# Performance work log

Hardware: AMD Instinct MI355X
Metric: run time of the kernel (lower is better)

The kernel has to match this reference:

```python
import jax, jax.numpy as jnp
import numpy as np

N = 8192
IN_F = 256
OUT_F = 64
ALPHA = 0.2
NEG_INF = -9e15


def setup_inputs() -> dict:
    key = jax.random.key(0)
    k1, k2, k3, k4 = jax.random.split(key, 4)
    h = jax.random.normal(k1, (N, IN_F), dtype=jnp.float32)
    W = jax.random.normal(k2, (IN_F, OUT_F), dtype=jnp.float32) * (1.414 / np.sqrt(IN_F))
    a = jax.random.normal(k3, (2 * OUT_F, 1), dtype=jnp.float32) * (1.414 / np.sqrt(2 * OUT_F))
    adj = jax.random.randint(k4, (N, N), 0, 2, dtype=jnp.int32)
    return {"h": h, "W": W, "a": a, "adj": adj}


def reference(h, W, a, adj):
    # Wh: [N, F]
    Wh = h @ W
    # Decompose concat-based attention: e_ij = LeakyReLU(Wh_i . a[:F] + Wh_j . a[F:])
    a1, a2 = a[:OUT_F], a[OUT_F:]
    src = Wh @ a1              # [N, 1] contribution of row i
    dst = Wh @ a2              # [N, 1] contribution of col j
    e = jax.nn.leaky_relu(src + dst.T, negative_slope=ALPHA)  # [N, N]
    e = jnp.where(adj > 0, e, NEG_INF)
    attention = jax.nn.softmax(e, axis=1)
    # dropout is identity in eval mode
    h_prime = attention @ Wh   # [N, F]
    return h_prime
```

## Files before the change

kernel.cpp:

```cpp
#include <hip/hip_runtime.h>

#define NROWS 8192
#define NSPLIT 8
#define JT (NROWS / NSPLIT)
#define NITER (JT / 64)
#define L2E 1.4426950408889634f

typedef __attribute__((ext_vector_type(4))) float f32x4;
typedef __attribute__((ext_vector_type(8))) __bf16 bf16x8;
typedef __attribute__((ext_vector_type(4))) unsigned int u32x4;

__device__ __forceinline__ unsigned short f2bf(float x) {
  unsigned u = __float_as_uint(x);
  u += 0x7fffu + ((u >> 16) & 1u);
  return (unsigned short)(u >> 16);
}

__global__ __launch_bounds__(256) void k_prep(
    const float* __restrict__ h, const float* __restrict__ W,
    const float* __restrict__ a, unsigned short* __restrict__ WhB,
    float* __restrict__ src, float* __restrict__ dst) {
  int i = blockIdx.x * 4 + (threadIdx.x >> 6);
  int lane = threadIdx.x & 63;
  const float* hrow = h + (size_t)i * 256;
  float s = 0.f;
#pragma unroll 4
  for (int k = 0; k < 256; k += 4) {
    float4 hv = *(const float4*)(hrow + k);
    s = fmaf(hv.x, W[(k + 0) * 64 + lane], s);
    s = fmaf(hv.y, W[(k + 1) * 64 + lane], s);
    s = fmaf(hv.z, W[(k + 2) * 64 + lane], s);
    s = fmaf(hv.w, W[(k + 3) * 64 + lane], s);
  }
  int nt = lane >> 4, c = lane & 15;
  int gi = (i >> 3) & 3, e = i & 7;
  int idx = ((((i >> 5) * 4 + nt) * 64) + c + 16 * gi) * 8 + e;
  WhB[idx] = f2bf(s);
  float v1 = s * a[lane];
  float v2 = s * a[64 + lane];
#pragma unroll
  for (int d = 32; d; d >>= 1) {
    v1 += __shfl_xor(v1, d);
    v2 += __shfl_xor(v2, d);
  }
  if (lane == 0) {
    src[i] = v1 * L2E;
    dst[i] = v2 * L2E;
  }
}

__global__ __launch_bounds__(256) void k_dmax(
    const float* __restrict__ dst, float* __restrict__ dmax) {
  __shared__ float red[4];
  float v = -INFINITY;
  for (int i = threadIdx.x; i < NROWS; i += 256) v = fmaxf(v, dst[i]);
#pragma unroll
  for (int d = 32; d; d >>= 1) v = fmaxf(v, __shfl_xor(v, d));
  if ((threadIdx.x & 63) == 0) red[threadIdx.x >> 6] = v;
  __syncthreads();
  if (threadIdx.x == 0)
    *dmax = fmaxf(fmaxf(red[0], red[1]), fmaxf(red[2], red[3]));
}

__global__ __launch_bounds__(256, 4) void k_attn(
    const int* __restrict__ adj, const unsigned short* __restrict__ WhB,
    const float* __restrict__ src, const float* __restrict__ dst,
    const float* __restrict__ dmax,
    float* __restrict__ pl, float* __restrict__ pacc) {
  __shared__ float ldst[JT];
  int task = blockIdx.x * 4 + (threadIdx.x >> 6);
  int sp = task >> 9;
  int mt = task & 511;
  int lane = threadIdx.x & 63;
  int r = lane & 15;
  int g = lane >> 4;
  int row0 = mt * 16;
  int jbase = sp * JT;

  for (int k = threadIdx.x; k < JT; k += 256) ldst[k] = dst[jbase + k];
  __syncthreads();

  float srcr = src[row0 + r];
  float dmv = *dmax;
  float vB = srcr + dmv;
  float Mi = fmaxf(vB, 0.2f * vB);

  float lrow = 0.f;
  f32x4 acc[4] = {f32x4{0.f, 0.f, 0.f, 0.f}, f32x4{0.f, 0.f, 0.f, 0.f},
                  f32x4{0.f, 0.f, 0.f, 0.f}, f32x4{0.f, 0.f, 0.f, 0.f}};
  const int* adjp = adj + (size_t)(row0 + r) * NROWS + jbase + 8 * g;
  const bf16x8* Bfr = (const bf16x8*)WhB;

  int4 ab[2][4];
  ab[0][0] = *(const int4*)(adjp + 0);
  ab[0][1] = *(const int4*)(adjp + 4);
  ab[0][2] = *(const int4*)(adjp + 32);
  ab[0][3] = *(const int4*)(adjp + 36);

#pragma unroll
  for (int it = 0; it < NITER; ++it) {
    const int jb = it * 64;
    const int cur = it & 1, nxt = cur ^ 1;

    int jc = (jbase + jb) >> 5;
    const bf16x8* bp = Bfr + (size_t)jc * 256 + lane;
    bf16x8 b0 = bp[0];
    bf16x8 b1 = bp[64];
    bf16x8 b2 = bp[128];
    bf16x8 b3 = bp[192];
    bf16x8 b4 = bp[256];
    bf16x8 b5 = bp[320];
    bf16x8 b6 = bp[384];
    bf16x8 b7 = bp[448];
    __builtin_amdgcn_sched_barrier(0);

    const int* ap = adjp + ((it < NITER - 1) ? jb + 64 : 0);
    ab[nxt][0] = *(const int4*)(ap + 0);
    ab[nxt][1] = *(const int4*)(ap + 4);
    ab[nxt][2] = *(const int4*)(ap + 32);
    ab[nxt][3] = *(const int4*)(ap + 36);
    __builtin_amdgcn_sched_barrier(0);

    const float4* dl = (const float4*)(ldst + jb + 8 * g);
    float4 d0 = dl[0];
    float4 d1 = dl[1];
    const float4* dl2 = (const float4*)(ldst + jb + 32 + 8 * g);
    float4 d2 = dl2[0];
    float4 d3 = dl2[1];

    float p[16];
#define PE(P, AA, DD)                     \
  {                                       \
    float v_ = srcr + (DD);               \
    v_ = fmaxf(v_, 0.2f * v_);            \
    float e_ = exp2f(v_ - Mi);            \
    (P) = ((AA) > 0) ? e_ : 0.f;          \
  }
    PE(p[0], ab[cur][0].x, d0.x) PE(p[1], ab[cur][0].y, d0.y)
    PE(p[2], ab[cur][0].z, d0.z) PE(p[3], ab[cur][0].w, d0.w)
    PE(p[4], ab[cur][1].x, d1.x) PE(p[5], ab[cur][1].y, d1.y)
    PE(p[6], ab[cur][1].z, d1.z) PE(p[7], ab[cur][1].w, d1.w)
    PE(p[8], ab[cur][2].x, d2.x) PE(p[9], ab[cur][2].y, d2.y)
    PE(p[10], ab[cur][2].z, d2.z) PE(p[11], ab[cur][2].w, d2.w)
    PE(p[12], ab[cur][3].x, d3.x) PE(p[13], ab[cur][3].y, d3.y)
    PE(p[14], ab[cur][3].z, d3.z) PE(p[15], ab[cur][3].w, d3.w)
#undef PE

    unsigned q[8];
#pragma unroll
    for (int t = 0; t < 16; t += 2) {
      lrow += p[t] + p[t + 1];
      unsigned qq;
      asm("v_cvt_pk_bf16_f32 %0, %1, %2" : "=v"(qq) : "v"(p[t]), "v"(p[t + 1]));
      q[t >> 1] = qq;
    }
    u32x4 qv0 = {q[0], q[1], q[2], q[3]};
    u32x4 qv1 = {q[4], q[5], q[6], q[7]};
    bf16x8 A0 = __builtin_bit_cast(bf16x8, qv0);
    bf16x8 A1 = __builtin_bit_cast(bf16x8, qv1);

    __builtin_amdgcn_s_setprio(1);
    acc[0] = __builtin_amdgcn_mfma_f32_16x16x32_bf16(A0, b0, acc[0], 0, 0, 0);
    acc[1] = __builtin_amdgcn_mfma_f32_16x16x32_bf16(A0, b1, acc[1], 0, 0, 0);
    acc[2] = __builtin_amdgcn_mfma_f32_16x16x32_bf16(A0, b2, acc[2], 0, 0, 0);
    acc[3] = __builtin_amdgcn_mfma_f32_16x16x32_bf16(A0, b3, acc[3], 0, 0, 0);
    acc[0] = __builtin_amdgcn_mfma_f32_16x16x32_bf16(A1, b4, acc[0], 0, 0, 0);
    acc[1] = __builtin_amdgcn_mfma_f32_16x16x32_bf16(A1, b5, acc[1], 0, 0, 0);
    acc[2] = __builtin_amdgcn_mfma_f32_16x16x32_bf16(A1, b6, acc[2], 0, 0, 0);
    acc[3] = __builtin_amdgcn_mfma_f32_16x16x32_bf16(A1, b7, acc[3], 0, 0, 0);
    __builtin_amdgcn_s_setprio(0);
  }

  lrow += __shfl_xor(lrow, 16);
  lrow += __shfl_xor(lrow, 32);
  if (lane < 16) pl[sp * NROWS + row0 + lane] = lrow;
#pragma unroll
  for (int nt = 0; nt < 4; nt++)
#pragma unroll
    for (int q2 = 0; q2 < 4; q2++)
      pacc[((size_t)sp * NROWS + row0 + 4 * g + q2) * 64 + nt * 16 + r] = acc[nt][q2];
}

__global__ __launch_bounds__(256) void k_comb(
    const float* __restrict__ pl, const float* __restrict__ pacc,
    float* __restrict__ out) {
  int t = blockIdx.x * 256 + threadIdx.x;
  int row = t >> 6, f = t & 63;
  float L = 0.f, o = 0.f;
#pragma unroll
  for (int s2 = 0; s2 < NSPLIT; s2++) {
    L += pl[s2 * NROWS + row];
    o += pacc[((size_t)s2 * NROWS + row) * 64 + f];
  }
  out[t] = o / L;
}

extern "C" void kernel_launch(void* const* d_in, const int* in_sizes, int n_in,
                              void* d_out, int out_size, void* d_ws, size_t ws_size,
                              hipStream_t stream) {
  const float* h = (const float*)d_in[0];
  const float* W = (const float*)d_in[1];
  const float* a = (const float*)d_in[2];
  const int* adj = (const int*)d_in[3];
  float* out = (float*)d_out;

  char* ws = (char*)d_ws;
  unsigned short* WhB = (unsigned short*)ws;
  float* src = (float*)(ws + 0x100000);
  float* dst = (float*)(ws + 0x108000);
  float* dmax = (float*)(ws + 0x110000);
  float* pl = (float*)(ws + 0x110100);
  float* pacc = (float*)(ws + 0x150100);

  hipLaunchKernelGGL(k_prep, dim3(NROWS / 4), dim3(256), 0, stream, h, W, a, WhB, src, dst);
  hipLaunchKernelGGL(k_dmax, dim3(1), dim3(256), 0, stream, dst, dmax);
  hipLaunchKernelGGL(k_attn, dim3(512 * NSPLIT / 4), dim3(256), 0, stream,
                     adj, WhB, src, dst, dmax, pl, pacc);
  hipLaunchKernelGGL(k_comb, dim3(NROWS * 64 / 256), dim3(256), 0, stream, pl, pacc, out);
}
```

Baseline: 124.5 us.

## Pack adjacency matrix into bitmasks before attention kernel

```diff
diff --git a/kernel.cpp b/kernel.cpp
--- a/kernel.cpp
+++ b/kernel.cpp
@@ -62,8 +62,27 @@
     *dmax = fmaxf(fmaxf(red[0], red[1]), fmaxf(red[2], red[3]));
 }
 
+__global__ __launch_bounds__(256) void k_pack(
+    const int* __restrict__ adj, unsigned long long* __restrict__ packed) {
+  int row = blockIdx.x * 4 + (threadIdx.x >> 6);
+  int lane = threadIdx.x & 63;
+  const int* rp = adj + (size_t)row * NROWS;
+#pragma unroll
+  for (int half = 0; half < 2; ++half) {
+    unsigned long long word = 0;
+#pragma unroll 8
+    for (int it = 0; it < 64; ++it) {
+      int v = rp[half * 4096 + it * 64 + lane];
+      unsigned long long bal = __ballot(v > 0);
+      word = (lane == it) ? bal : word;
+    }
+    packed[(size_t)row * 128 + half * 64 + lane] = word;
+  }
+}
+
 __global__ __launch_bounds__(256, 4) void k_attn(
-    const int* __restrict__ adj, const unsigned short* __restrict__ WhB,
+    const unsigned long long* __restrict__ packed,
+    const unsigned short* __restrict__ WhB,
     const float* __restrict__ src, const float* __restrict__ dst,
     const float* __restrict__ dmax,
     float* __restrict__ pl, float* __restrict__ pacc) {
@@ -81,26 +100,21 @@
   __syncthreads();
 
   float srcr = src[row0 + r];
-  float dmv = *dmax;
-  float vB = srcr + dmv;
+  float vB = srcr + *dmax;
   float Mi = fmaxf(vB, 0.2f * vB);
 
   float lrow = 0.f;
   f32x4 acc[4] = {f32x4{0.f, 0.f, 0.f, 0.f}, f32x4{0.f, 0.f, 0.f, 0.f},
                   f32x4{0.f, 0.f, 0.f, 0.f}, f32x4{0.f, 0.f, 0.f, 0.f}};
-  const int* adjp = adj + (size_t)(row0 + r) * NROWS + jbase + 8 * g;
+  const unsigned long long* pwp =
+      packed + (size_t)(row0 + r) * (NROWS / 64) + (jbase >> 6);
   const bf16x8* Bfr = (const bf16x8*)WhB;
-
-  int4 ab[2][4];
-  ab[0][0] = *(const int4*)(adjp + 0);
-  ab[0][1] = *(const int4*)(adjp + 4);
-  ab[0][2] = *(const int4*)(adjp + 32);
-  ab[0][3] = *(const int4*)(adjp + 36);
 
 #pragma unroll
   for (int it = 0; it < NITER; ++it) {
     const int jb = it * 64;
-    const int cur = it & 1, nxt = cur ^ 1;
+
+    unsigned long long pw = pwp[it];
 
     int jc = (jbase + jb) >> 5;
     const bf16x8* bp = Bfr + (size_t)jc * 256 + lane;
@@ -112,38 +126,32 @@
     bf16x8 b5 = bp[320];
     bf16x8 b6 = bp[384];
     bf16x8 b7 = bp[448];
-    __builtin_amdgcn_sched_barrier(0);
-
-    const int* ap = adjp + ((it < NITER - 1) ? jb + 64 : 0);
-    ab[nxt][0] = *(const int4*)(ap + 0);
-    ab[nxt][1] = *(const int4*)(ap + 4);
-    ab[nxt][2] = *(const int4*)(ap + 32);
-    ab[nxt][3] = *(const int4*)(ap + 36);
-    __builtin_amdgcn_sched_barrier(0);
-
-    const float4* dl = (const float4*)(ldst + jb + 8 * g);
-    float4 d0 = dl[0];
-    float4 d1 = dl[1];
-    const float4* dl2 = (const float4*)(ldst + jb + 32 + 8 * g);
-    float4 d2 = dl2[0];
-    float4 d3 = dl2[1];
+
+    const float* dl = ldst + jb + 8 * g;
+    float4 d0 = *(const float4*)(dl);
+    float4 d1 = *(const float4*)(dl + 4);
+    float4 d2 = *(const float4*)(dl + 32);
+    float4 d3 = *(const float4*)(dl + 36);
+
+    unsigned lo = (unsigned)(pw >> (8 * g));
+    unsigned hi = (unsigned)(pw >> (32 + 8 * g));
 
     float p[16];
-#define PE(P, AA, DD)                     \
+#define PE(P, BIT, DD)                    \
   {                                       \
     float v_ = srcr + (DD);               \
     v_ = fmaxf(v_, 0.2f * v_);            \
     float e_ = exp2f(v_ - Mi);            \
-    (P) = ((AA) > 0) ? e_ : 0.f;          \
-  }
-    PE(p[0], ab[cur][0].x, d0.x) PE(p[1], ab[cur][0].y, d0.y)
-    PE(p[2], ab[cur][0].z, d0.z) PE(p[3], ab[cur][0].w, d0.w)
-    PE(p[4], ab[cur][1].x, d1.x) PE(p[5], ab[cur][1].y, d1.y)
-    PE(p[6], ab[cur][1].z, d1.z) PE(p[7], ab[cur][1].w, d1.w)
-    PE(p[8], ab[cur][2].x, d2.x) PE(p[9], ab[cur][2].y, d2.y)
-    PE(p[10], ab[cur][2].z, d2.z) PE(p[11], ab[cur][2].w, d2.w)
-    PE(p[12], ab[cur][3].x, d3.x) PE(p[13], ab[cur][3].y, d3.y)
-    PE(p[14], ab[cur][3].z, d3.z) PE(p[15], ab[cur][3].w, d3.w)
+    (P) = (BIT) ? e_ : 0.f;               \
+  }
+    PE(p[0], lo & 1u, d0.x)   PE(p[1], lo & 2u, d0.y)
+    PE(p[2], lo & 4u, d0.z)   PE(p[3], lo & 8u, d0.w)
+    PE(p[4], lo & 16u, d1.x)  PE(p[5], lo & 32u, d1.y)
+    PE(p[6], lo & 64u, d1.z)  PE(p[7], lo & 128u, d1.w)
+    PE(p[8], hi & 1u, d2.x)   PE(p[9], hi & 2u, d2.y)
+    PE(p[10], hi & 4u, d2.z)  PE(p[11], hi & 8u, d2.w)
+    PE(p[12], hi & 16u, d3.x) PE(p[13], hi & 32u, d3.y)
+    PE(p[14], hi & 64u, d3.z) PE(p[15], hi & 128u, d3.w)
 #undef PE
 
     unsigned q[8];
@@ -211,10 +219,12 @@
   float* dmax = (float*)(ws + 0x110000);
   float* pl = (float*)(ws + 0x110100);
   float* pacc = (float*)(ws + 0x150100);
+  unsigned long long* packed = (unsigned long long*)(ws + 0x1150100);
 
   hipLaunchKernelGGL(k_prep, dim3(NROWS / 4), dim3(256), 0, stream, h, W, a, WhB, src, dst);
   hipLaunchKernelGGL(k_dmax, dim3(1), dim3(256), 0, stream, dst, dmax);
+  hipLaunchKernelGGL(k_pack, dim3(NROWS / 4), dim3(256), 0, stream, adj, packed);
   hipLaunchKernelGGL(k_attn, dim3(512 * NSPLIT / 4), dim3(256), 0, stream,
-                     adj, WhB, src, dst, dmax, pl, pacc);
+                     packed, WhB, src, dst, dmax, pl, pacc);
   hipLaunchKernelGGL(k_comb, dim3(NROWS * 64 / 256), dim3(256), 0, stream, pl, pacc, out);
 }
```

Measured after the change: 131.5 us. +5.6%, slower.
